# Kernel optimization log

Measured on AMD Instinct MI355X. Metric: run time of the kernel, lower is better.

## Reference

```python
import jax, jax.numpy as jnp
import numpy as np

N_ATOMS = 100_000
N_BONDS = 200_000
MAX_NB = 6
ATOM_FDIM = 133
BOND_FDIM = 147
HIDDEN = 256
DEPTH = 5
ATOMS_PER_MOL = 100


def setup_inputs() -> dict:
    key = jax.random.key(0)
    ks = jax.random.split(key, 9)
    f_atoms = jax.random.normal(ks[0], (N_ATOMS, ATOM_FDIM), dtype=jnp.float32)
    f_bonds = jax.random.normal(ks[1], (N_BONDS, BOND_FDIM), dtype=jnp.float32)
    a2b = jax.random.randint(ks[2], (N_ATOMS, MAX_NB), 0, N_BONDS, dtype=jnp.int32)
    b2a = jax.random.randint(ks[3], (N_BONDS,), 0, N_ATOMS, dtype=jnp.int32)
    # reverse bond of 2i is 2i+1 and vice versa (chemprop directed-bond pairing)
    b2revb = (jnp.arange(N_BONDS, dtype=jnp.int32) ^ 1)
    s_i = 1.0 / np.sqrt(BOND_FDIM)
    s_h = 1.0 / np.sqrt(HIDDEN)
    s_o = 1.0 / np.sqrt(ATOM_FDIM + HIDDEN)
    W_i = jax.random.uniform(ks[4], (HIDDEN, BOND_FDIM), jnp.float32, -s_i, s_i)
    W_h = jax.random.uniform(ks[5], (HIDDEN, HIDDEN), jnp.float32, -s_h, s_h)
    W_o = jax.random.uniform(ks[6], (HIDDEN, ATOM_FDIM + HIDDEN), jnp.float32, -s_o, s_o)
    b_o = jax.random.uniform(ks[7], (HIDDEN,), jnp.float32, -s_o, s_o)
    return {"f_atoms": f_atoms, "f_bonds": f_bonds, "a2b": a2b, "b2a": b2a,
            "b2revb": b2revb, "W_i": W_i, "W_h": W_h, "W_o": W_o, "b_o": b_o,
            "atoms_per_mol": ATOMS_PER_MOL}


def reference(f_atoms, f_bonds, a2b, b2a, b2revb, W_i, W_h, W_o, b_o, atoms_per_mol):
    # input = W_i(f_bonds); message = relu(input)   [n_bonds, H]
    inp = jnp.einsum('bf,hf->bh', f_bonds, W_i)
    message = jax.nn.relu(inp)
    for _ in range(DEPTH - 1):
        # gather incoming-bond messages per atom and sum: [n_atoms, max_nb, H] -> [n_atoms, H]
        a_message = message[a2b].sum(axis=1)
        # directed-MPNN update: subtract reverse-bond message
        m = a_message[b2a] - message[b2revb]
        message = jax.nn.relu(inp + jnp.einsum('bh,gh->bg', m, W_h))
        # dropout p=0.0 (eval) -> identity
    a_message = message[a2b].sum(axis=1)                      # [n_atoms, H]
    a_input = jnp.concatenate([f_atoms, a_message], axis=1)   # [n_atoms, atom_fdim+H]
    atom_hiddens = jax.nn.relu(jnp.einsum('af,hf->ah', a_input, W_o) + b_o)
    # uniform a_scope: stack per-molecule atom blocks -> [n_mols, atoms_per_mol, H]
    return atom_hiddens.reshape(-1, atoms_per_mol, HIDDEN)
```

## Files before the change

### kernel.cpp

```cpp
#include <hip/hip_runtime.h>
#include <hip/hip_bf16.h>

typedef unsigned short u16;
typedef unsigned short u16x8 __attribute__((ext_vector_type(8)));
typedef short s8vec __attribute__((ext_vector_type(8)));
typedef float f4vec __attribute__((ext_vector_type(4)));

__device__ __forceinline__ float bf2f(u16 u) {
    union { unsigned int i; float f; } c; c.i = ((unsigned int)u) << 16; return c.f;
}
__device__ __forceinline__ u16 f2bf(float f) {
    union { float f; unsigned int i; } c; c.f = f;
    unsigned int x = c.i;
    x += 0x7fffu + ((x >> 16) & 1u);
    return (u16)(x >> 16);
}
__device__ __forceinline__ void gload_lds16(const void* g, void* l) {
    __builtin_amdgcn_global_load_lds((__attribute__((address_space(1))) void*)g,
                                     (__attribute__((address_space(3))) void*)l, 16, 0, 0);
}
__device__ __forceinline__ int sw4(int r) { return (r + (r >> 2)) & 3; }

__global__ void pad_w_all(const float* __restrict__ W_i, const float* __restrict__ W_h,
                          const float* __restrict__ W_o,
                          u16* __restrict__ Wi, u16* __restrict__ Wh,
                          u16* __restrict__ Wo2, u16* __restrict__ Wo1) {
    int r = blockIdx.x;
    int which = blockIdx.y;
    const float* src; u16* dst; int sstride, col0, nvalid, dcol;
    if (which == 0)      { src = W_i; dst = Wi;  sstride = 147; col0 = 0;   nvalid = 147; dcol = 192; }
    else if (which == 1) { src = W_h; dst = Wh;  sstride = 256; col0 = 0;   nvalid = 256; dcol = 256; }
    else if (which == 2) { src = W_o; dst = Wo2; sstride = 389; col0 = 133; nvalid = 256; dcol = 256; }
    else                 { src = W_o; dst = Wo1; sstride = 389; col0 = 0;   nvalid = 133; dcol = 192; }
    for (int c = threadIdx.x; c < dcol; c += blockDim.x) {
        float v = (c < nvalid) ? src[(size_t)r * sstride + col0 + c] : 0.f;
        dst[(size_t)r * dcol + c] = f2bf(v);
    }
}

__global__ void gather6_kernel(const u16* __restrict__ P, const int* __restrict__ a2b,
                               u16* __restrict__ out, int n_atoms) {
    int lane = threadIdx.x & 63;
    int half = lane >> 5;
    int col = (lane & 31) * 8;
    int wid = (blockIdx.x * blockDim.x + threadIdx.x) >> 6;
    int nw = (gridDim.x * blockDim.x) >> 6;
    for (int a0 = wid * 2; a0 < n_atoms; a0 += nw * 2) {
        int a = a0 + half;
        float acc[8];
#pragma unroll
        for (int e = 0; e < 8; ++e) acc[e] = 0.f;
#pragma unroll
        for (int j = 0; j < 6; ++j) {
            int b = a2b[a * 6 + j];
            u16x8 v = *(const u16x8*)(P + (size_t)b * 256 + col);
#pragma unroll
            for (int e = 0; e < 8; ++e) acc[e] += bf2f(v[e]);
        }
        u16x8 o;
#pragma unroll
        for (int e = 0; e < 8; ++e) o[e] = f2bf(acc[e]);
        *(u16x8*)(out + (size_t)a * 256 + col) = o;
    }
}

template <int ASTAGE, int EPI>
__launch_bounds__(256, 4)
__global__ void gemm256_kernel(const void* __restrict__ Asrc, const u16* __restrict__ Pm,
                               const u16* __restrict__ aPm, const int* __restrict__ b2a,
                               const u16* __restrict__ Bw, int M, int Kp, int scol, int nk,
                               void* __restrict__ out0, const u16* __restrict__ aQ,
                               const float* __restrict__ bias) {
    __shared__ __align__(16) char smem[2][20480];
    const int t = threadIdx.x;
    const int w = t >> 6, lane = t & 63;
    const int row0 = blockIdx.x * 64;

    const int ar = t >> 2;
    const int aslot = t & 3;
    int grow = row0 + ar; if (grow >= M) grow = M - 1;
    const int aphys = aslot ^ sw4(ar);
    int nbrow = 0;
    if (ASTAGE == 4) nbrow = b2a[grow];

    f4vec acc[4][4];
#pragma unroll
    for (int i = 0; i < 4; ++i)
#pragma unroll
        for (int j = 0; j < 4; ++j) acc[i][j] = (f4vec){0.f, 0.f, 0.f, 0.f};

    u16x8 rv0, rv1, rv2;
    float rs[8];

    auto stageA_load = [&](int k0) {
        int coff = k0 + aslot * 8;
        if (ASTAGE == 1) {
            const float* src = (const float*)Asrc + (size_t)grow * scol;
#pragma unroll
            for (int e = 0; e < 8; ++e)
                rs[e] = (coff + e < scol) ? src[coff + e] : 0.f;
        } else if (ASTAGE == 2) {
            rv0 = *(const u16x8*)((const u16*)Asrc + (size_t)grow * 256 + coff);
        } else {
            rv0 = *(const u16x8*)((const u16*)Asrc + (size_t)grow * 256 + coff);
            rv1 = *(const u16x8*)(Pm + (size_t)(grow ^ 1) * 256 + coff);
            rv2 = *(const u16x8*)(aPm + (size_t)nbrow * 256 + coff);
        }
    };
    auto stageA_write = [&](int buf) {
        u16x8 v;
        if (ASTAGE == 1) {
#pragma unroll
            for (int e = 0; e < 8; ++e) v[e] = f2bf(rs[e]);
        } else if (ASTAGE == 2) {
#pragma unroll
            for (int e = 0; e < 8; ++e) v[e] = (rv0[e] >> 15) ? (u16)0 : rv0[e];
        } else {
#pragma unroll
            for (int e = 0; e < 8; ++e)
                v[e] = f2bf(fmaxf(bf2f(rv0[e]) + bf2f(rv2[e]) - bf2f(rv1[e]), 0.f));
        }
        *(u16x8*)&smem[buf][ar * 64 + aphys * 16] = v;
    };
    auto stageB = [&](int buf, int k0) {
#pragma unroll
        for (int i = 0; i < 4; ++i) {
            int rlin = (w * 4 + i) * 16 + (lane >> 2);
            int chunk = (lane & 3) ^ sw4(rlin);
            const u16* gp = Bw + (size_t)rlin * Kp + k0 + chunk * 8;
            gload_lds16(gp, &smem[buf][4096 + (w * 4 + i) * 1024]);
        }
    };
    auto compute = [&](int buf) {
        s8vec af[4], bfr[4];
#pragma unroll
        for (int i = 0; i < 4; ++i) {
            int r = i * 16 + (lane & 15);
            int p = (lane >> 4) ^ sw4(r);
            af[i] = *(const s8vec*)&smem[buf][r * 64 + p * 16];
        }
#pragma unroll
        for (int j = 0; j < 4; ++j) {
            int c = w * 64 + j * 16 + (lane & 15);
            int p = (lane >> 4) ^ sw4(c);
            bfr[j] = *(const s8vec*)&smem[buf][4096 + c * 64 + p * 16];
        }
#pragma unroll
        for (int i = 0; i < 4; ++i)
#pragma unroll
            for (int j = 0; j < 4; ++j)
                acc[i][j] = __builtin_amdgcn_mfma_f32_16x16x32_bf16(af[i], bfr[j], acc[i][j], 0, 0, 0);
    };

    stageA_load(0);
    stageB(0, 0);
    stageA_write(0);
    __syncthreads();
    int cur = 0;
    for (int ks = 0; ks < nk; ++ks) {
        if (ks + 1 < nk) {
            stageA_load((ks + 1) * 32);
            stageB(cur ^ 1, (ks + 1) * 32);
        }
        compute(cur);
        if (ks + 1 < nk) stageA_write(cur ^ 1);
        __syncthreads();
        cur ^= 1;
    }

#pragma unroll
    for (int i = 0; i < 4; ++i) {
        int Rbase = row0 + i * 16 + (lane >> 4) * 4;
#pragma unroll
        for (int j = 0; j < 4; ++j) {
            int C = w * 64 + j * 16 + (lane & 15);
#pragma unroll
            for (int r = 0; r < 4; ++r) {
                int R = Rbase + r;
                if (R < M) {
                    float v = acc[i][j][r];
                    if (EPI == 0) {
                        ((u16*)out0)[(size_t)R * 256 + C] = f2bf(v);
                    } else {
                        float o = v + bf2f(aQ[(size_t)R * 256 + C]) + bias[C];
                        ((float*)out0)[(size_t)R * 256 + C] = fmaxf(o, 0.f);
                    }
                }
            }
        }
    }
}

extern "C" void kernel_launch(void* const* d_in, const int* in_sizes, int n_in,
                              void* d_out, int out_size, void* d_ws, size_t ws_size,
                              hipStream_t stream) {
    const float* f_atoms = (const float*)d_in[0];
    const float* f_bonds = (const float*)d_in[1];
    const int* a2b = (const int*)d_in[2];
    const int* b2a = (const int*)d_in[3];
    const float* W_i = (const float*)d_in[5];
    const float* W_h = (const float*)d_in[6];
    const float* W_o = (const float*)d_in[7];
    const float* b_o = (const float*)d_in[8];

    const int NA = 100000, NB = 200000;

    char* ws = (char*)d_ws;
    u16* inp = (u16*)(ws + 0);
    u16* Pa  = (u16*)(ws + 102400000);
    u16* Pb  = (u16*)(ws + 204800000);
    u16* aP  = (u16*)(ws + 307200000);
    u16* Wi  = (u16*)(ws + 358400000);
    u16* Wh  = (u16*)(ws + 358498304);
    u16* Wo2 = (u16*)(ws + 358629376);
    u16* Wo1 = (u16*)(ws + 358760448);
    if (ws_size < 358858752u) return;

    pad_w_all<<<dim3(256, 4), dim3(256), 0, stream>>>(W_i, W_h, W_o, Wi, Wh, Wo2, Wo1);

    const int GB = NB / 64;
    const int GA = (NA + 63) / 64;

    gemm256_kernel<1, 0><<<dim3(GB), dim3(256), 0, stream>>>(
        f_bonds, nullptr, nullptr, nullptr, Wi, NB, 192, 147, 6, inp, nullptr, nullptr);

    gemm256_kernel<2, 0><<<dim3(GB), dim3(256), 0, stream>>>(
        inp, nullptr, nullptr, nullptr, Wh, NB, 256, 0, 8, Pa, nullptr, nullptr);
    gather6_kernel<<<dim3(2048), dim3(256), 0, stream>>>(Pa, a2b, aP, NA);

    u16* Pcur = Pa; u16* Pnxt = Pb;
    for (int it = 0; it < 3; ++it) {
        gemm256_kernel<4, 0><<<dim3(GB), dim3(256), 0, stream>>>(
            inp, Pcur, aP, b2a, Wh, NB, 256, 0, 8, Pnxt, nullptr, nullptr);
        gather6_kernel<<<dim3(2048), dim3(256), 0, stream>>>(Pnxt, a2b, aP, NA);
        u16* tmp = Pcur; Pcur = Pnxt; Pnxt = tmp;
    }

    gemm256_kernel<4, 0><<<dim3(GB), dim3(256), 0, stream>>>(
        inp, Pcur, aP, b2a, Wo2, NB, 256, 0, 8, Pnxt, nullptr, nullptr);
    gather6_kernel<<<dim3(2048), dim3(256), 0, stream>>>(Pnxt, a2b, aP, NA);

    gemm256_kernel<1, 3><<<dim3(GA), dim3(256), 0, stream>>>(
        f_atoms, nullptr, nullptr, nullptr, Wo1, NA, 192, 133, 6, d_out, aP, b_o);
}
```

Measured before the change: 887.4 us.

## Replace tiled GEMM with persistent kernel keeping whole weight matrix in LDS

The double-buffered 64-row GEMM is replaced by a persistent kernel. Each 512-thread block loads the full swizzled bf16 weight matrix into LDS once, up to 128KB. Each wave then independently streams RF*16-row tiles, loading A fragments straight from global into registers with the relu/message-combine fused in, and runs MFMAs across all 256 output columns. This removes per-K-step weight reloads and block-wide barriers, at the cost of large LDS use (one block per CU), many accumulator registers, and per-wave global A loads with no LDS staging.

After: 1.357 ms. +52.9%, slower.

```diff
diff --git a/kernel.cpp b/kernel.cpp
--- a/kernel.cpp
+++ b/kernel.cpp
@@ -19,7 +19,6 @@
     __builtin_amdgcn_global_load_lds((__attribute__((address_space(1))) void*)g,
                                      (__attribute__((address_space(3))) void*)l, 16, 0, 0);
 }
-__device__ __forceinline__ int sw4(int r) { return (r + (r >> 2)) & 3; }
 
 __global__ void pad_w_all(const float* __restrict__ W_i, const float* __restrict__ W_h,
                           const float* __restrict__ W_o,
@@ -64,125 +63,104 @@
     }
 }
 
-template <int ASTAGE, int EPI>
-__launch_bounds__(256, 4)
-__global__ void gemm256_kernel(const void* __restrict__ Asrc, const u16* __restrict__ Pm,
-                               const u16* __restrict__ aPm, const int* __restrict__ b2a,
-                               const u16* __restrict__ Bw, int M, int Kp, int scol, int nk,
-                               void* __restrict__ out0, const u16* __restrict__ aQ,
-                               const float* __restrict__ bias) {
-    __shared__ __align__(16) char smem[2][20480];
+template <int ASTAGE, int EPI, int KP, int RF>
+__launch_bounds__(512, 2)
+__global__ void gemm_stream(const void* __restrict__ Asrc, const u16* __restrict__ Pm,
+                            const u16* __restrict__ aPm, const int* __restrict__ b2a,
+                            const u16* __restrict__ Bw, int M, int scol,
+                            void* __restrict__ out0, const u16* __restrict__ aQ,
+                            const float* __restrict__ bias) {
+    constexpr int CPR = KP / 8;
+    constexpr int NKS = KP / 32;
+    constexpr int TR = RF * 16;
+    __shared__ __align__(16) char smem[256 * KP * 2];
+
     const int t = threadIdx.x;
     const int w = t >> 6, lane = t & 63;
-    const int row0 = blockIdx.x * 64;
-
-    const int ar = t >> 2;
-    const int aslot = t & 3;
-    int grow = row0 + ar; if (grow >= M) grow = M - 1;
-    const int aphys = aslot ^ sw4(ar);
-    int nbrow = 0;
-    if (ASTAGE == 4) nbrow = b2a[grow];
-
-    f4vec acc[4][4];
-#pragma unroll
-    for (int i = 0; i < 4; ++i)
-#pragma unroll
-        for (int j = 0; j < 4; ++j) acc[i][j] = (f4vec){0.f, 0.f, 0.f, 0.f};
-
-    u16x8 rv0, rv1, rv2;
-    float rs[8];
-
-    auto stageA_load = [&](int k0) {
-        int coff = k0 + aslot * 8;
-        if (ASTAGE == 1) {
-            const float* src = (const float*)Asrc + (size_t)grow * scol;
-#pragma unroll
-            for (int e = 0; e < 8; ++e)
-                rs[e] = (coff + e < scol) ? src[coff + e] : 0.f;
-        } else if (ASTAGE == 2) {
-            rv0 = *(const u16x8*)((const u16*)Asrc + (size_t)grow * 256 + coff);
-        } else {
-            rv0 = *(const u16x8*)((const u16*)Asrc + (size_t)grow * 256 + coff);
-            rv1 = *(const u16x8*)(Pm + (size_t)(grow ^ 1) * 256 + coff);
-            rv2 = *(const u16x8*)(aPm + (size_t)nbrow * 256 + coff);
-        }
-    };
-    auto stageA_write = [&](int buf) {
-        u16x8 v;
-        if (ASTAGE == 1) {
-#pragma unroll
-            for (int e = 0; e < 8; ++e) v[e] = f2bf(rs[e]);
-        } else if (ASTAGE == 2) {
-#pragma unroll
-            for (int e = 0; e < 8; ++e) v[e] = (rv0[e] >> 15) ? (u16)0 : rv0[e];
-        } else {
-#pragma unroll
-            for (int e = 0; e < 8; ++e)
-                v[e] = f2bf(fmaxf(bf2f(rv0[e]) + bf2f(rv2[e]) - bf2f(rv1[e]), 0.f));
-        }
-        *(u16x8*)&smem[buf][ar * 64 + aphys * 16] = v;
-    };
-    auto stageB = [&](int buf, int k0) {
-#pragma unroll
-        for (int i = 0; i < 4; ++i) {
-            int rlin = (w * 4 + i) * 16 + (lane >> 2);
-            int chunk = (lane & 3) ^ sw4(rlin);
-            const u16* gp = Bw + (size_t)rlin * Kp + k0 + chunk * 8;
-            gload_lds16(gp, &smem[buf][4096 + (w * 4 + i) * 1024]);
-        }
-    };
-    auto compute = [&](int buf) {
-        s8vec af[4], bfr[4];
-#pragma unroll
-        for (int i = 0; i < 4; ++i) {
-            int r = i * 16 + (lane & 15);
-            int p = (lane >> 4) ^ sw4(r);
-            af[i] = *(const s8vec*)&smem[buf][r * 64 + p * 16];
-        }
-#pragma unroll
-        for (int j = 0; j < 4; ++j) {
-            int c = w * 64 + j * 16 + (lane & 15);
-            int p = (lane >> 4) ^ sw4(c);
-            bfr[j] = *(const s8vec*)&smem[buf][4096 + c * 64 + p * 16];
-        }
-#pragma unroll
-        for (int i = 0; i < 4; ++i)
-#pragma unroll
-            for (int j = 0; j < 4; ++j)
-                acc[i][j] = __builtin_amdgcn_mfma_f32_16x16x32_bf16(af[i], bfr[j], acc[i][j], 0, 0, 0);
-    };
-
-    stageA_load(0);
-    stageB(0, 0);
-    stageA_write(0);
+    const int ln15 = lane & 15, hi = lane >> 4;
+
+    constexpr int ITER = (256 * CPR) / 512;
+#pragma unroll
+    for (int i = 0; i < ITER; ++i) {
+        int d = i * 512 + t;
+        int row = d / CPR, pc = d % CPR;
+        int c = pc ^ (row & 7);
+        gload_lds16(Bw + (size_t)row * KP + c * 8, &smem[(size_t)(i * 512 + w * 64) * 16]);
+    }
     __syncthreads();
-    int cur = 0;
-    for (int ks = 0; ks < nk; ++ks) {
-        if (ks + 1 < nk) {
-            stageA_load((ks + 1) * 32);
-            stageB(cur ^ 1, (ks + 1) * 32);
-        }
-        compute(cur);
-        if (ks + 1 < nk) stageA_write(cur ^ 1);
-        __syncthreads();
-        cur ^= 1;
-    }
-
-#pragma unroll
-    for (int i = 0; i < 4; ++i) {
-        int Rbase = row0 + i * 16 + (lane >> 4) * 4;
-#pragma unroll
-        for (int j = 0; j < 4; ++j) {
-            int C = w * 64 + j * 16 + (lane & 15);
-#pragma unroll
-            for (int r = 0; r < 4; ++r) {
-                int R = Rbase + r;
-                if (R < M) {
-                    float v = acc[i][j][r];
+
+    const int ntiles = M / TR;
+    const int nw = gridDim.x * 8;
+    for (int tile = blockIdx.x * 8 + w; tile < ntiles; tile += nw) {
+        const int r0 = tile * TR;
+
+        u16x8 a[RF][NKS];
+#pragma unroll
+        for (int rf = 0; rf < RF; ++rf) {
+            const int gr = r0 + rf * 16 + ln15;
+            int nb = 0;
+            if (ASTAGE == 4) nb = b2a[gr];
+#pragma unroll
+            for (int ks = 0; ks < NKS; ++ks) {
+                const int coff = ks * 32 + hi * 8;
+                u16x8 v;
+                if (ASTAGE == 1) {
+                    const float* src = (const float*)Asrc + (size_t)gr * scol;
+#pragma unroll
+                    for (int e = 0; e < 8; ++e) {
+                        float x = 0.f;
+                        if (coff + e < scol) x = src[coff + e];
+                        v[e] = f2bf(x);
+                    }
+                } else if (ASTAGE == 2) {
+                    u16x8 x = *(const u16x8*)((const u16*)Asrc + (size_t)gr * 256 + coff);
+#pragma unroll
+                    for (int e = 0; e < 8; ++e) v[e] = (x[e] >> 15) ? (u16)0 : x[e];
+                } else {
+                    u16x8 vi = *(const u16x8*)((const u16*)Asrc + (size_t)gr * 256 + coff);
+                    u16x8 vp = *(const u16x8*)(Pm + (size_t)(gr ^ 1) * 256 + coff);
+                    u16x8 va = *(const u16x8*)(aPm + (size_t)nb * 256 + coff);
+#pragma unroll
+                    for (int e = 0; e < 8; ++e)
+                        v[e] = f2bf(fmaxf(bf2f(vi[e]) + bf2f(va[e]) - bf2f(vp[e]), 0.f));
+                }
+                a[rf][ks] = v;
+            }
+        }
+
+        f4vec acc[RF][16];
+#pragma unroll
+        for (int rf = 0; rf < RF; ++rf)
+#pragma unroll
+            for (int j = 0; j < 16; ++j) acc[rf][j] = (f4vec){0.f, 0.f, 0.f, 0.f};
+
+        const int bb = ln15 * (CPR * 16);
+#pragma unroll
+        for (int ks = 0; ks < NKS; ++ks) {
+            const int pco = (((ks * 4 + hi) ^ (ln15 & 7))) * 16;
+#pragma unroll
+            for (int j = 0; j < 16; ++j) {
+                s8vec bf = *(const s8vec*)&smem[j * (CPR * 256) + bb + pco];
+#pragma unroll
+                for (int rf = 0; rf < RF; ++rf)
+                    acc[rf][j] = __builtin_amdgcn_mfma_f32_16x16x32_bf16(
+                        *(const s8vec*)&a[rf][ks], bf, acc[rf][j], 0, 0, 0);
+            }
+        }
+
+#pragma unroll
+        for (int rf = 0; rf < RF; ++rf) {
+#pragma unroll
+            for (int j = 0; j < 16; ++j) {
+                const int C = j * 16 + ln15;
+#pragma unroll
+                for (int r = 0; r < 4; ++r) {
+                    const int R = r0 + rf * 16 + hi * 4 + r;
+                    float vv = acc[rf][j][r];
                     if (EPI == 0) {
-                        ((u16*)out0)[(size_t)R * 256 + C] = f2bf(v);
+                        ((u16*)out0)[(size_t)R * 256 + C] = f2bf(vv);
                     } else {
-                        float o = v + bf2f(aQ[(size_t)R * 256 + C]) + bias[C];
+                        float o = vv + bf2f(aQ[(size_t)R * 256 + C]) + bias[C];
                         ((float*)out0)[(size_t)R * 256 + C] = fmaxf(o, 0.f);
                     }
                 }
@@ -218,28 +196,25 @@
 
     pad_w_all<<<dim3(256, 4), dim3(256), 0, stream>>>(W_i, W_h, W_o, Wi, Wh, Wo2, Wo1);
 
-    const int GB = NB / 64;
-    const int GA = (NA + 63) / 64;
-
-    gemm256_kernel<1, 0><<<dim3(GB), dim3(256), 0, stream>>>(
-        f_bonds, nullptr, nullptr, nullptr, Wi, NB, 192, 147, 6, inp, nullptr, nullptr);
-
-    gemm256_kernel<2, 0><<<dim3(GB), dim3(256), 0, stream>>>(
-        inp, nullptr, nullptr, nullptr, Wh, NB, 256, 0, 8, Pa, nullptr, nullptr);
+    gemm_stream<1, 0, 192, 1><<<dim3(512), dim3(512), 0, stream>>>(
+        f_bonds, nullptr, nullptr, nullptr, Wi, NB, 147, inp, nullptr, nullptr);
+
+    gemm_stream<2, 0, 256, 2><<<dim3(512), dim3(512), 0, stream>>>(
+        inp, nullptr, nullptr, nullptr, Wh, NB, 0, Pa, nullptr, nullptr);
     gather6_kernel<<<dim3(2048), dim3(256), 0, stream>>>(Pa, a2b, aP, NA);
 
     u16* Pcur = Pa; u16* Pnxt = Pb;
     for (int it = 0; it < 3; ++it) {
-        gemm256_kernel<4, 0><<<dim3(GB), dim3(256), 0, stream>>>(
-            inp, Pcur, aP, b2a, Wh, NB, 256, 0, 8, Pnxt, nullptr, nullptr);
+        gemm_stream<4, 0, 256, 2><<<dim3(512), dim3(512), 0, stream>>>(
+            inp, Pcur, aP, b2a, Wh, NB, 0, Pnxt, nullptr, nullptr);
         gather6_kernel<<<dim3(2048), dim3(256), 0, stream>>>(Pnxt, a2b, aP, NA);
         u16* tmp = Pcur; Pcur = Pnxt; Pnxt = tmp;
     }
 
-    gemm256_kernel<4, 0><<<dim3(GB), dim3(256), 0, stream>>>(
-        inp, Pcur, aP, b2a, Wo2, NB, 256, 0, 8, Pnxt, nullptr, nullptr);
+    gemm_stream<4, 0, 256, 2><<<dim3(512), dim3(512), 0, stream>>>(
+        inp, Pcur, aP, b2a, Wo2, NB, 0, Pnxt, nullptr, nullptr);
     gather6_kernel<<<dim3(2048), dim3(256), 0, stream>>>(Pnxt, a2b, aP, NA);
 
-    gemm256_kernel<1, 3><<<dim3(GA), dim3(256), 0, stream>>>(
-        f_atoms, nullptr, nullptr, nullptr, Wo1, NA, 192, 133, 6, d_out, aP, b_o);
-}
+    gemm_stream<1, 3, 192, 1><<<dim3(512), dim3(512), 0, stream>>>(
+        f_atoms, nullptr, nullptr, nullptr, Wo1, NA, 133, d_out, aP, b_o);
+}
```
